# Performance work log

Hardware: AMD Instinct MI355X
Metric: run time of the kernel (lower is better)

Reference implementation:

```python
import jax, jax.numpy as jnp
import numpy as np

N_NODES = 20000
N_EDGES = 320000
MUL = 64            # multiplicity of 0e and 1o node irreps
N_SPECIES = 5
N_BESSEL = 8
RAD_HIDDEN = 64
N_TP_W = 4 * MUL    # 4 uvu paths, 64 weights each
AVG_NEIGH = 16.0
SQ3 = np.sqrt(3.0).astype(np.float32)


def setup_inputs() -> dict:
    key = jax.random.key(0)
    ks = jax.random.split(key, 16)
    inp = {
        'node_feats': jax.random.normal(ks[0], (N_NODES, 4 * MUL), jnp.float32),
        'node_attrs': jax.random.uniform(ks[1], (N_NODES, N_SPECIES), jnp.float32),
        'edge_sh': jax.random.normal(ks[2], (N_EDGES, 4), jnp.float32),
        'senders': jax.random.randint(ks[3], (N_EDGES,), 0, N_NODES),
        'receivers': jax.random.randint(ks[4], (N_EDGES,), 0, N_NODES),
        'edge_embedded': jax.random.normal(ks[5], (N_EDGES, N_BESSEL), jnp.float32),
        # Linear on node feats (per-irrep mixing): 64x0e->64x0e, 64x1o->64x1o
        'Wl0': jax.random.normal(ks[6], (MUL, MUL), jnp.float32),
        'Wl1': jax.random.normal(ks[7], (MUL, MUL), jnp.float32),
        # radial MLP: 8 -> 64 -> 64 -> 256, no bias, scalar_mlp_std = 4.0
        'Wm1': jax.random.normal(ks[8], (N_BESSEL, RAD_HIDDEN), jnp.float32) * 4.0,
        'Wm2': jax.random.normal(ks[9], (RAD_HIDDEN, RAD_HIDDEN), jnp.float32) * 4.0,
        'Wm3': jax.random.normal(ks[10], (RAD_HIDDEN, N_TP_W), jnp.float32) * 4.0,
        # output Linear: (128x0e + 128x1o after TP) -> h_out (128x0e + 64x1o)
        'W2s': jax.random.normal(ks[11], (2 * MUL, 2 * MUL), jnp.float32),
        'W2v': jax.random.normal(ks[12], (2 * MUL, MUL), jnp.float32),
        # residual FullyConnectedTensorProduct(node_feats, node_attrs) -> h_out
        'Wr_s': jax.random.normal(ks[13], (MUL, N_SPECIES, 2 * MUL), jnp.float32),
        'Wr_v': jax.random.normal(ks[14], (MUL, N_SPECIES, MUL), jnp.float32),
    }
    return inp


def reference(node_feats, node_attrs, edge_sh, senders, receivers, edge_embedded,
              Wl0, Wl1, Wm1, Wm2, Wm3, W2s, W2v, Wr_s, Wr_v):
    N = node_feats.shape[0]
    x0 = node_feats[:, :MUL]                       # [N, 64]   0e scalars
    x1 = node_feats[:, MUL:].reshape(N, MUL, 3)    # [N, 64, 3] 1o vectors

    # --- residual FullyConnectedTensorProduct(node_feats, node_attrs) -> h_out ---
    # node_attrs are 0e scalars: paths 0e x 0e -> 0e and 1o x 0e -> 1o.
    nr = 1.0 / np.sqrt(MUL * N_SPECIES).astype(np.float32)  # fan-in norm
    res_s = jnp.einsum('nu,ns,usv->nv', x0, node_attrs, Wr_s) * nr   # [N, 128]
    res_v = jnp.einsum('num,ns,usv->nvm', x1, node_attrs, Wr_v) * nr # [N, 64, 3]

    # --- Linear(node_feats.irreps) ---
    nl = 1.0 / np.sqrt(MUL).astype(np.float32)
    y0 = (x0 @ Wl0) * nl                                  # [N, 64]
    y1 = jnp.einsum('num,uv->nvm', x1, Wl1) * nl          # [N, 64, 3]

    # --- gather to edges ---
    e0 = y0[senders]          # [E, 64]
    e1 = y1[senders]          # [E, 64, 3]
    sh0 = edge_sh[:, 0]       # [E]
    sh1 = edge_sh[:, 1:4]     # [E, 3]

    # --- radial MLP producing per-edge TP weights ---
    h = jax.nn.swish(edge_embedded @ Wm1 / np.sqrt(N_BESSEL, dtype=np.float32))
    h = jax.nn.swish(h @ Wm2 / np.sqrt(RAD_HIDDEN, dtype=np.float32))
    w = h @ Wm3 / np.sqrt(RAD_HIDDEN, dtype=np.float32)   # [E, 256]
    w1, w2, w3, w4 = (w[:, :MUL], w[:, MUL:2*MUL], w[:, 2*MUL:3*MUL], w[:, 3*MUL:])

    # --- equivariant tensor product (uvu), 4 paths ---
    # 0e x 0e -> 0e ; 1o x 1o -> 0e (CG = delta/sqrt(3))
    tp_s = jnp.concatenate([
        w1 * e0 * sh0[:, None],
        w4 * jnp.einsum('eum,em->eu', e1, sh1) / SQ3,
    ], axis=1)  # [E, 128]
    # 0e x 1o -> 1o ; 1o x 0e -> 1o
    tp_v = jnp.concatenate([
        w2[:, :, None] * e0[:, :, None] * sh1[:, None, :],
        w3[:, :, None] * e1 * sh0[:, None, None],
    ], axis=1)  # [E, 128, 3]

    # --- scatter-sum aggregation over receivers ---
    agg_s = jax.ops.segment_sum(tp_s, receivers, num_segments=N) / AVG_NEIGH          # [N, 128]
    agg_v = jax.ops.segment_sum(tp_v.reshape(-1, 2 * MUL * 3), receivers,
                                num_segments=N).reshape(N, 2 * MUL, 3) / AVG_NEIGH    # [N, 128, 3]

    # --- Linear(h_out_irreps) ---
    n2 = 1.0 / np.sqrt(2 * MUL).astype(np.float32)
    z_s = (agg_s @ W2s) * n2                               # [N, 128] (64 scalars + 64 gates)
    z_v = jnp.einsum('num,uv->nvm', agg_v, W2v) * n2       # [N, 64, 3]

    # residual connection
    z_s = z_s + res_s
    z_v = z_v + res_v

    # --- gate: even_act = swish on scalars and gate scalars; gated 1o vectors ---
    out_s = jax.nn.swish(z_s[:, :MUL])                     # [N, 64]
    gates = jax.nn.swish(z_s[:, MUL:])                     # [N, 64]
    out_v = gates[:, :, None] * z_v                        # [N, 64, 3]

    return jnp.concatenate([out_s, out_v.reshape(N, MUL * 3)], axis=1)  # [N, 256]
```

## Files before the change

### kernel.cpp

```cpp
#include <hip/hip_runtime.h>
#include <hip/hip_fp16.h>


#define NN 20000
#define NE 320000

typedef _Float16 h2v __attribute__((ext_vector_type(2)));
typedef _Float16 f16x8 __attribute__((ext_vector_type(8)));
typedef float f32x4 __attribute__((ext_vector_type(4)));

__device__ __forceinline__ float swishf(float x) {
  float t = __expf(-fabsf(x));
  float r = 1.0f / (1.0f + t);
  float sig = (x >= 0.0f) ? r : t * r;
  return x * sig;
}

__device__ __forceinline__ unsigned pack2h(float a, float b) {
  __half2 h = __floats2half2_rn(a, b);
  return *reinterpret_cast<unsigned*>(&h);
}

__device__ __forceinline__ h2v u32h2(unsigned u) {
  union { unsigned u; h2v h; } x; x.u = u; return x.h;
}

__device__ __forceinline__ h2v packh2v(float a, float b) {
  h2v h; h.x = (_Float16)a; h.y = (_Float16)b; return h;
}

__device__ __forceinline__ f16x8 u4f16(uint4 u) {
  union { uint4 u; f16x8 h; } x; x.u = u; return x.h;
}

__device__ __forceinline__ void ld8(float d[8], const float* p) {
  float4 a0 = *(const float4*)p;
  float4 a1 = *(const float4*)(p + 4);
  d[0]=a0.x; d[1]=a0.y; d[2]=a0.z; d[3]=a0.w;
  d[4]=a1.x; d[5]=a1.y; d[6]=a1.z; d[7]=a1.w;
}

__device__ __forceinline__ void fma8v(float (&acc)[8], const float* p, float w) {
  float4 a0 = *(const float4*)p;
  float4 a1 = *(const float4*)(p + 4);
  acc[0] = fmaf(a0.x, w, acc[0]); acc[1] = fmaf(a0.y, w, acc[1]);
  acc[2] = fmaf(a0.z, w, acc[2]); acc[3] = fmaf(a0.w, w, acc[3]);
  acc[4] = fmaf(a1.x, w, acc[4]); acc[5] = fmaf(a1.y, w, acc[5]);
  acc[6] = fmaf(a1.z, w, acc[6]); acc[7] = fmaf(a1.w, w, acc[7]);
}

__global__ __launch_bounds__(256) void hist_kernel(const int* __restrict__ rcv,
                                                   int* __restrict__ counts) {
  int e = blockIdx.x * 256 + threadIdx.x;
  atomicAdd(&counts[rcv[e]], 1);
}

__global__ __launch_bounds__(1024) void scan_kernel(const int* __restrict__ counts,
                                                    int* __restrict__ offsets,
                                                    int* __restrict__ cursor) {
  __shared__ int part[1024];
  const int t = threadIdx.x;
  const int base = t * 20;
  int loc[20];
  int s = 0;
  #pragma unroll
  for (int j = 0; j < 20; ++j) {
    int idx = base + j;
    int c = (idx < NN) ? counts[idx] : 0;
    loc[j] = s;
    s += c;
  }
  part[t] = s;
  __syncthreads();
  for (int d = 1; d < 1024; d <<= 1) {
    int v = (t >= d) ? part[t - d] : 0;
    __syncthreads();
    part[t] += v;
    __syncthreads();
  }
  int excl = (t > 0) ? part[t - 1] : 0;
  #pragma unroll
  for (int j = 0; j < 20; ++j) {
    int idx = base + j;
    if (idx < NN) {
      int o = excl + loc[j];
      offsets[idx] = o;
      cursor[idx] = o;
    }
  }
  if (t == 1023) offsets[NN] = part[1023];
}

__global__ __launch_bounds__(256) void scatter_full(
    const int* __restrict__ rcv, const int* __restrict__ snd,
    const float* __restrict__ esh, int* __restrict__ cursor,
    int* __restrict__ csr_edge, int* __restrict__ snd_sorted,
    float* __restrict__ sh_sorted) {
  int e = blockIdx.x * 256 + threadIdx.x;
  int r = rcv[e];
  int pos = atomicAdd(&cursor[r], 1);
  csr_edge[pos] = e;
  snd_sorted[pos] = snd[e];
  float4 sh = *(const float4*)(esh + (size_t)e * 4);
  *(float4*)(sh_sorted + (size_t)pos * 4) = sh;
}

__global__ __launch_bounds__(256) void scatter_kernel(
    const int* __restrict__ rcv, int* __restrict__ cursor,
    int* __restrict__ csr_edge) {
  int e = blockIdx.x * 256 + threadIdx.x;
  int r = rcv[e];
  int pos = atomicAdd(&cursor[r], 1);
  csr_edge[pos] = e;
}

__global__ __launch_bounds__(256) void pack_weights(
    const float* __restrict__ Wm2, const float* __restrict__ Wm3,
    unsigned* __restrict__ Wm2P, unsigned* __restrict__ Wm3P,
    unsigned* __restrict__ Wm3T) {
  int idx = blockIdx.x * 256 + threadIdx.x;
  if (idx < 2048) {
    int k2 = idx >> 6, v = idx & 63;
    Wm2P[idx] = pack2h(Wm2[(2 * k2) * 64 + v], Wm2[(2 * k2 + 1) * 64 + v]);
  } else if (idx < 10240) {
    int r = idx - 2048;
    int k2 = r >> 8, c = r & 255;
    Wm3P[r] = pack2h(Wm3[(2 * k2) * 256 + c], Wm3[(2 * k2 + 1) * 256 + c]);
  } else if (idx < 18432) {
    int r = idx - 10240;
    int c = r >> 5, j = r & 31;
    Wm3T[r] = pack2h(Wm3[(2 * j) * 256 + c], Wm3[(2 * j + 1) * 256 + c]);
  }
}

__global__ __launch_bounds__(256) void pack_node_B(
    const float* __restrict__ Wr_s, const float* __restrict__ W2s,
    const float* __restrict__ Wr_v, const float* __restrict__ W2v,
    unsigned* __restrict__ BsT, unsigned* __restrict__ BvT) {
  const float nr = 0.05590169943749474f;
  const float n2 = 0.08838834764831845f;
  int idx = blockIdx.x * 256 + threadIdx.x;
  if (idx < 28672) {
    int v = idx / 224, j = idx % 224;
    float a, b;
    if (j < 160) {
      int s = j >> 5, u0 = (j & 31) << 1;
      a = Wr_s[(u0 * 5 + s) * 128 + v] * nr;
      b = Wr_s[((u0 + 1) * 5 + s) * 128 + v] * nr;
    } else {
      int c0 = (j - 160) << 1;
      a = W2s[c0 * 128 + v] * n2;
      b = W2s[(c0 + 1) * 128 + v] * n2;
    }
    BsT[idx] = pack2h(a, b);
  } else if (idx < 43008) {
    int r = idx - 28672;
    int v = r / 224, j = r % 224;
    float a, b;
    if (j < 160) {
      int s = j >> 5, u0 = (j & 31) << 1;
      a = Wr_v[(u0 * 5 + s) * 64 + v] * nr;
      b = Wr_v[((u0 + 1) * 5 + s) * 64 + v] * nr;
    } else {
      int c0 = (j - 160) << 1;
      a = W2v[c0 * 64 + v] * n2;
      b = W2v[(c0 + 1) * 64 + v] * n2;
    }
    BvT[r] = pack2h(a, b);
  }
}

__global__ __launch_bounds__(256) void node_prep(
    const float* __restrict__ feats, const float* __restrict__ Wl0,
    const float* __restrict__ Wl1, float* __restrict__ y)
{
  __shared__ __align__(16) float sX[4 * 256];
  const int t = threadIdx.x;
  const int n0 = blockIdx.x * 4;
  #pragma unroll
  for (int nb = 0; nb < 4; ++nb)
    sX[nb * 256 + t] = feats[(size_t)(n0 + nb) * 256 + t];
  __syncthreads();

  float acc[4] = {0.f, 0.f, 0.f, 0.f};
  if (t < 64) {
    const int v = t;
    for (int u = 0; u < 64; ++u) {
      float w = Wl0[u * 64 + v];
      acc[0] = fmaf(sX[0 * 256 + u], w, acc[0]);
      acc[1] = fmaf(sX[1 * 256 + u], w, acc[1]);
      acc[2] = fmaf(sX[2 * 256 + u], w, acc[2]);
      acc[3] = fmaf(sX[3 * 256 + u], w, acc[3]);
    }
  } else {
    const int i = t - 64;
    const int v = i / 3;
    const int m = i - v * 3;
    for (int u = 0; u < 64; ++u) {
      float w = Wl1[u * 64 + v];
      int xi = 64 + u * 3 + m;
      acc[0] = fmaf(sX[0 * 256 + xi], w, acc[0]);
      acc[1] = fmaf(sX[1 * 256 + xi], w, acc[1]);
      acc[2] = fmaf(sX[2 * 256 + xi], w, acc[2]);
      acc[3] = fmaf(sX[3 * 256 + xi], w, acc[3]);
    }
  }
  #pragma unroll
  for (int nb = 0; nb < 4; ++nb)
    y[(size_t)(n0 + nb) * 256 + t] = acc[nb] * 0.125f;
}

__device__ __forceinline__ void wgemv(float (&wa)[64], const float* __restrict__ Wm3,
                                      const float* h2col, int p)
{
  #pragma unroll
  for (int v = 0; v < 64; ++v) wa[v] = 0.f;
  #pragma unroll 2
  for (int k = 0; k < 64; ++k) {
    float h2k = h2col[k * 256];
    const float* wrow = Wm3 + k * 256 + p * 64;
    #pragma unroll
    for (int v = 0; v < 64; ++v) wa[v] = fmaf(h2k, wrow[v], wa[v]);
  }
}

__global__ __launch_bounds__(256, 4) void w_kernel(
    const int* __restrict__ csr_edge, const float* __restrict__ emb,
    const float* __restrict__ Wm1, const unsigned* __restrict__ Wm2P,
    const unsigned* __restrict__ Wm3T, __half* __restrict__ w_sorted)
{
  __shared__ unsigned sA[256 * 32];
  const int tid = threadIdx.x;
  const int i = blockIdx.x * 256 + tid;
  const int e = csr_edge[i];

  float e8[8];
  ld8(e8, emb + (size_t)e * 8);
  float h2a[64];
  #pragma unroll
  for (int v = 0; v < 64; ++v) h2a[v] = 0.f;
  #pragma unroll 1
  for (int k2 = 0; k2 < 32; ++k2) {
    float a0 = 0.f, a1 = 0.f;
    #pragma unroll
    for (int j = 0; j < 8; ++j) {
      a0 = fmaf(e8[j], Wm1[j * 64 + 2 * k2], a0);
      a1 = fmaf(e8[j], Wm1[j * 64 + 2 * k2 + 1], a1);
    }
    h2v ph = packh2v(swishf(a0 * 0.35355339059327373f),
                     swishf(a1 * 0.35355339059327373f));
    const unsigned* wrow = Wm2P + k2 * 64;
    #pragma unroll
    for (int v = 0; v < 64; ++v)
      h2a[v] = __builtin_amdgcn_fdot2(ph, u32h2(wrow[v]), h2a[v], false);
  }
  {
    const int r = tid;
    #pragma unroll
    for (int c = 0; c < 8; ++c) {
      uint4 v;
      v.x = pack2h(swishf(h2a[8 * c + 0] * 0.125f), swishf(h2a[8 * c + 1] * 0.125f));
      v.y = pack2h(swishf(h2a[8 * c + 2] * 0.125f), swishf(h2a[8 * c + 3] * 0.125f));
      v.z = pack2h(swishf(h2a[8 * c + 4] * 0.125f), swishf(h2a[8 * c + 5] * 0.125f));
      v.w = pack2h(swishf(h2a[8 * c + 6] * 0.125f), swishf(h2a[8 * c + 7] * 0.125f));
      *(uint4*)&sA[r * 32 + ((c ^ (r & 7)) << 2)] = v;
    }
  }
  __syncthreads();

  const int l = tid & 63;
  const int wv = tid >> 6;
  const int lg = l >> 4;
  const int lm = l & 15;

  f16x8 bfr[4][2];
  #pragma unroll
  for (int nt = 0; nt < 4; ++nt) {
    int row = wv * 64 + nt * 16 + lm;
    #pragma unroll
    for (int kh = 0; kh < 2; ++kh) {
      uint4 u = *(const uint4*)&sA[row * 32 + ((((kh << 2) + lg) ^ (row & 7)) << 2)];
      bfr[nt][kh] = u4f16(u);
    }
  }
  unsigned* sTw = sA + wv * 2048;
  const int eb = blockIdx.x * 256 + wv * 64;

  #pragma unroll 1
  for (int p = 0; p < 4; ++p) {
    #pragma unroll
    for (int mtl = 0; mtl < 4; ++mtl) {
      const int mt = p * 4 + mtl;
      int arow = mt * 16 + lm;
      uint4 u0 = *(const uint4*)&Wm3T[arow * 32 + (lg << 2)];
      uint4 u1 = *(const uint4*)&Wm3T[arow * 32 + 16 + (lg << 2)];
      f16x8 a0 = u4f16(u0), a1 = u4f16(u1);
      #pragma unroll
      for (int nt = 0; nt < 4; ++nt) {
        f32x4 acc = {0.f, 0.f, 0.f, 0.f};
        acc = __builtin_amdgcn_mfma_f32_16x16x32_f16(a0, bfr[nt][0], acc, 0, 0, 0);
        acc = __builtin_amdgcn_mfma_f32_16x16x32_f16(a1, bfr[nt][1], acc, 0, 0, 0);
        const int r = nt * 16 + lm;
        const int u = mtl * 4 + lg;
        const int pos8 = ((((u >> 1) ^ (r & 7)) << 1) | (u & 1));
        uint2 pk;
        pk.x = pack2h(acc[0], acc[1]);
        pk.y = pack2h(acc[2], acc[3]);
        *(uint2*)&sTw[r * 32 + pos8 * 2] = pk;
      }
    }
    #pragma unroll
    for (int g = 0; g < 8; ++g) {
      const int er = g * 8 + (l >> 3);
      const int c8 = l & 7;
      uint4 v = *(const uint4*)&sTw[er * 32 + ((c8 ^ (er & 7)) << 2)];
      *(uint4*)(w_sorted + (size_t)(eb + er) * 256 + p * 64 + c8 * 8) = v;
    }
  }
}

__global__ __launch_bounds__(256) void gather_tp(
    const float* __restrict__ y, const __half* __restrict__ w_sorted,
    const float* __restrict__ sh_sorted, const int* __restrict__ snd_sorted,
    const int* __restrict__ offsets, float* __restrict__ agg)
{
  const int l = threadIdx.x & 63;
  const int wv = threadIdx.x >> 6;
  const int n = blockIdx.x * 4 + wv;
  const int row0 = offsets[n];
  const int row1 = offsets[n + 1];

  float s0 = 0.f, s1 = 0.f;
  float v0x = 0.f, v0y = 0.f, v0z = 0.f;
  float v1x = 0.f, v1y = 0.f, v1z = 0.f;

  for (int i = row0; i < row1; ++i) {
    const int s = snd_sorted[i];
    const float4 sh = *(const float4*)(sh_sorted + (size_t)i * 4);
    const __half* wr = w_sorted + (size_t)i * 256;
    float w1 = __half2float(wr[l]);
    float w2 = __half2float(wr[64 + l]);
    float w3 = __half2float(wr[128 + l]);
    float w4 = __half2float(wr[192 + l]);
    const float* yr = y + (size_t)s * 256;
    float e0 = yr[l];
    float ex = yr[64 + 3 * l], ey = yr[65 + 3 * l], ez = yr[66 + 3 * l];

    s0 = fmaf(w1 * e0, sh.x, s0);
    s1 = fmaf(w4, fmaf(ex, sh.y, fmaf(ey, sh.z, ez * sh.w)), s1);
    float t2 = w2 * e0;
    v0x = fmaf(t2, sh.y, v0x); v0y = fmaf(t2, sh.z, v0y); v0z = fmaf(t2, sh.w, v0z);
    float t3 = w3 * sh.x;
    v1x = fmaf(t3, ex, v1x); v1y = fmaf(t3, ey, v1y); v1z = fmaf(t3, ez, v1z);
  }

  const float SCL = 0.0078125f;
  const float C4  = 0.125f / (16.0f * 1.7320508075688772f);
  float* ar = agg + (size_t)n * 512;
  ar[l]       = s0 * SCL;
  ar[64 + l]  = s1 * C4;
  ar[128 + 3 * l]     = v0x * SCL;
  ar[128 + 3 * l + 1] = v0y * SCL;
  ar[128 + 3 * l + 2] = v0z * SCL;
  ar[320 + 3 * l]     = v1x * SCL;
  ar[320 + 3 * l + 1] = v1y * SCL;
  ar[320 + 3 * l + 2] = v1z * SCL;
}

__global__ __launch_bounds__(256) void node_gemm(
    const float* __restrict__ feats, const float* __restrict__ attrs,
    const float* __restrict__ agg, const unsigned* __restrict__ BsT,
    const unsigned* __restrict__ BvT, float* __restrict__ out)
{
  __shared__ unsigned sAK[64 * 224];
  __shared__ float sX[16 * 257];
  __shared__ float sAt[16 * 5];
  const int t = threadIdx.x;
  const int n0 = blockIdx.x * 16;

  float* zsL = sX;
  __half* zvL = (__half*)(sX + 2048);

  #pragma unroll
  for (int nb = 0; nb < 16; ++nb)
    sX[nb * 257 + t] = feats[(size_t)(n0 + nb) * 256 + t];
  if (t < 80) sAt[t] = attrs[(size_t)n0 * 5 + t];
  __syncthreads();

  {
    const int row = t >> 2;
    const int part = t & 3;
    const bool is_s = row < 16;
    int node, m = 0;
    if (is_s) node = row;
    else { int vi = row - 16; node = vi / 3; m = vi - node * 3; }
    const float* xrow = &sX[node * 257];
    const float* atr = &sAt[node * 5];
    const float* aggr = agg + (size_t)(n0 + node) * 512;
    unsigned* arow = &sAK[row * 224];
    #pragma unroll 8
    for (int jj = 0; jj < 56; ++jj) {
      const int j = part + 4 * jj;
      float v0, v1;
      if (jj < 40) {
        int s = j >> 5;
        int u0 = (j & 31) << 1;
        float a = atr[s];
        float x0 = is_s ? xrow[u0]     : xrow[64 + 3 * u0 + m];
        float x1 = is_s ? xrow[u0 + 1] : xrow[64 + 3 * u0 + 3 + m];
        v0 = x0 * a;
        v1 = x1 * a;
      } else {
        int c0 = (j - 160) << 1;
        if (is_s) { v0 = aggr[c0]; v1 = aggr[c0 + 1]; }
        else {
          v0 = aggr[128 + 3 * c0 + m];
          v1 = aggr[128 + 3 * c0 + 3 + m];
        }
      }
      int chs = (jj & ~7) | ((jj ^ row) & 7);
      arow[(chs << 2) + part] = pack2h(v0, v1);
    }
  }
  __syncthreads();

  const int l = t & 63;
  const int wv = t >> 6;
  const int lm = l & 15;
  const int lg = l >> 4;

  #pragma unroll 1
  for (int jj = 0; jj < 5; ++jj) {
    const int jd = wv + 4 * jj;
    int mtile, ntile;
    const unsigned* Bt;
    if (jd < 8) { mtile = 0; ntile = jd; Bt = BsT; }
    else { int q = jd - 8; mtile = 1 + (q >> 2); ntile = q & 3; Bt = BvT; }

    const int arow0 = mtile * 16 + lm;
    const unsigned* brow = Bt + (ntile * 16 + lm) * 224;

    uint4 ubr[14];
    #pragma unroll
    for (int ks = 0; ks < 14; ++ks)
      ubr[ks] = *(const uint4*)&brow[(ks * 4 + lg) << 2];

    f32x4 acc = {0.f, 0.f, 0.f, 0.f};
    #pragma unroll
    for (int ks = 0; ks < 14; ++ks) {
      int ch = ks * 4 + lg;
      int chs = (ch & ~7) | ((ch ^ arow0) & 7);
      uint4 ua = *(const uint4*)&sAK[arow0 * 224 + (chs << 2)];
      acc = __builtin_amdgcn_mfma_f32_16x16x32_f16(u4f16(ua), u4f16(ubr[ks]), acc, 0, 0, 0);
    }
    const int drow = mtile * 16 + lg * 4;
    if (jd < 8) {
      #pragma unroll
      for (int rr = 0; rr < 4; ++rr)
        zsL[(drow + rr) * 128 + ntile * 16 + lm] = acc[rr];
    } else {
      const int vi0 = drow - 16;
      #pragma unroll
      for (int rr = 0; rr < 4; ++rr)
        zvL[(vi0 + rr) * 64 + ntile * 16 + lm] = __float2half(acc[rr]);
    }
  }
  __syncthreads();

  int ug = 0, mg = 0;
  if (t >= 64) { ug = (t - 64) / 3; mg = (t - 64) - ug * 3; }
  #pragma unroll 4
  for (int nb = 0; nb < 16; ++nb) {
    float val;
    if (t < 64) {
      val = swishf(zsL[nb * 128 + t]);
    } else {
      float gate = swishf(zsL[nb * 128 + 64 + ug]);
      val = gate * __half2float(zvL[(nb * 3 + mg) * 64 + ug]);
    }
    out[(size_t)(n0 + nb) * 256 + t] = val;
  }
}

__global__ __launch_bounds__(512, 2) void gather_fused(
    const float* __restrict__ y, const int* __restrict__ csr_edge,
    const int* __restrict__ snd, const float* __restrict__ esh,
    const float* __restrict__ emb, const float* __restrict__ Wm1,
    const float* __restrict__ Wm2, const float* __restrict__ Wm3,
    const int* __restrict__ offsets, float* __restrict__ agg)
{
  __shared__ __align__(16) float sW3[64 * 256];
  __shared__ __align__(16) float sH[8 * 4 * 64];
  const int t = threadIdx.x;

  #pragma unroll 4
  for (int i = 0; i < 32; ++i) {
    int idx = i * 512 + t;
    int k = idx >> 8;
    int c = idx & 255;
    float v = Wm3[idx];
    int kg = k >> 2, kk = k & 3;
    sW3[c * 64 + (((kg ^ (c & 15)) & 15) << 2) + kk] = v;
  }
  __syncthreads();

  const int l = t & 63;
  const int wv = t >> 6;
  const int n = blockIdx.x * 8 + wv;
  const int row0 = offsets[n];
  const int row1 = offsets[n + 1];

  float* sHw = &sH[wv * 256];

  float wm1r[8];
  #pragma unroll
  for (int j = 0; j < 8; ++j) wm1r[j] = Wm1[j * 64 + l];

  float s0 = 0.f, s1 = 0.f;
  float v0x = 0.f, v0y = 0.f, v0z = 0.f;
  float v1x = 0.f, v1y = 0.f, v1z = 0.f;

  const int swz = ((l & 15) << 2);

  for (int i = row0; i < row1; i += 4) {
    const int nb = row1 - i;

    int   sn[4];
    float4 sh[4];
    #pragma unroll
    for (int b = 0; b < 4; ++b) {
      int idx = (b < nb) ? (i + b) : i;
      int e = csr_edge[idx];
      sn[b] = snd[e];
      float4 s = *(const float4*)(esh + (size_t)e * 4);
      if (b >= nb) s = make_float4(0.f, 0.f, 0.f, 0.f);
      sh[b] = s;
      float em8[8];
      ld8(em8, emb + (size_t)e * 8);
      float a = 0.f;
      #pragma unroll
      for (int j = 0; j < 8; ++j) a = fmaf(em8[j], wm1r[j], a);
      sHw[b * 64 + l] = swishf(a * 0.35355339059327373f);
    }

    float h2[4] = {0.f, 0.f, 0.f, 0.f};
    #pragma unroll 4
    for (int q = 0; q < 16; ++q) {
      float wq0 = Wm2[(4 * q + 0) * 64 + l];
      float wq1 = Wm2[(4 * q + 1) * 64 + l];
      float wq2 = Wm2[(4 * q + 2) * 64 + l];
      float wq3 = Wm2[(4 * q + 3) * 64 + l];
      #pragma unroll
      for (int b = 0; b < 4; ++b) {
        float4 h = *(const float4*)&sHw[b * 64 + 4 * q];
        h2[b] = fmaf(h.x, wq0, h2[b]);
        h2[b] = fmaf(h.y, wq1, h2[b]);
        h2[b] = fmaf(h.z, wq2, h2[b]);
        h2[b] = fmaf(h.w, wq3, h2[b]);
      }
    }
    #pragma unroll
    for (int b = 0; b < 4; ++b)
      h2[b] = swishf(h2[b] * 0.125f);
    #pragma unroll
    for (int b = 0; b < 4; ++b)
      sHw[b * 64 + l] = h2[b];

    float w0[4]  = {0,0,0,0}, w1a[4] = {0,0,0,0};
    float w2a[4] = {0,0,0,0}, w3a[4] = {0,0,0,0};
    #pragma unroll 1
    for (int g = 0; g < 16; ++g) {
      int sbase = l * 64 + (((g << 2) ^ swz) & 63);
      float4 m0 = *(const float4*)&sW3[sbase];
      float4 m1 = *(const float4*)&sW3[sbase + 4096];
      float4 m2 = *(const float4*)&sW3[sbase + 8192];
      float4 m3 = *(const float4*)&sW3[sbase + 12288];
      #pragma unroll
      for (int b = 0; b < 4; ++b) {
        float4 hb = *(const float4*)&sHw[b * 64 + 4 * g];
        #pragma unroll
        for (int kk = 0; kk < 4; ++kk) {
          float bc = (&hb.x)[kk];
          w0[b]  = fmaf(bc, (&m0.x)[kk], w0[b]);
          w1a[b] = fmaf(bc, (&m1.x)[kk], w1a[b]);
          w2a[b] = fmaf(bc, (&m2.x)[kk], w2a[b]);
          w3a[b] = fmaf(bc, (&m3.x)[kk], w3a[b]);
        }
      }
    }

    #pragma unroll
    for (int b = 0; b < 4; ++b) {
      const float* yr = y + (size_t)sn[b] * 256;
      float e0 = yr[l];
      float ex = yr[64 + 3 * l], ey = yr[65 + 3 * l], ez = yr[66 + 3 * l];
      float4 s = sh[b];
      s0 = fmaf(w0[b] * e0, s.x, s0);
      s1 = fmaf(w3a[b], fmaf(ex, s.y, fmaf(ey, s.z, ez * s.w)), s1);
      float t2 = w1a[b] * e0;
      v0x = fmaf(t2, s.y, v0x); v0y = fmaf(t2, s.z, v0y); v0z = fmaf(t2, s.w, v0z);
      float t3 = w2a[b] * s.x;
      v1x = fmaf(t3, ex, v1x); v1y = fmaf(t3, ey, v1y); v1z = fmaf(t3, ez, v1z);
    }
  }

  const float SCL = 0.0078125f;
  const float C4  = 0.125f / (16.0f * 1.7320508075688772f);
  float* ar = agg + (size_t)n * 512;
  ar[l]       = s0 * SCL;
  ar[64 + l]  = s1 * C4;
  ar[128 + 3 * l]     = v0x * SCL;
  ar[128 + 3 * l + 1] = v0y * SCL;
  ar[128 + 3 * l + 2] = v0z * SCL;
  ar[320 + 3 * l]     = v1x * SCL;
  ar[320 + 3 * l + 1] = v1y * SCL;
  ar[320 + 3 * l + 2] = v1z * SCL;
}

__global__ __launch_bounds__(256) void edge_kernel(
    const float* __restrict__ y, const float* __restrict__ edge_sh,
    const int* __restrict__ senders, const int* __restrict__ receivers,
    const float* __restrict__ emb, const float* __restrict__ Wm1,
    const float* __restrict__ Wm2, const float* __restrict__ Wm3,
    float* __restrict__ agg)
{
  __shared__ float h2s[64 * 256];
  const int tid = threadIdx.x;
  const int e = blockIdx.x * 256 + tid;
  const int s = senders[e];
  const int r = receivers[e];
  const float4 shv = *(const float4*)(edge_sh + (size_t)e * 4);
  float e8[8];
  ld8(e8, emb + (size_t)e * 8);

  float h2a[64];
  #pragma unroll
  for (int v = 0; v < 64; ++v) h2a[v] = 0.f;
  #pragma unroll 2
  for (int k = 0; k < 64; ++k) {
    float a = 0.f;
    #pragma unroll
    for (int j = 0; j < 8; ++j) a = fmaf(e8[j], Wm1[j * 64 + k], a);
    float h1k = swishf(a * 0.35355339059327373f);
    const float* wrow = Wm2 + k * 64;
    #pragma unroll
    for (int v = 0; v < 64; ++v) h2a[v] = fmaf(h1k, wrow[v], h2a[v]);
  }
  #pragma unroll
  for (int v = 0; v < 64; ++v)
    h2s[v * 256 + tid] = swishf(h2a[v] * 0.125f);

  const float* yrow = y + (size_t)s * 256;
  float* aggr = agg + (size_t)r * 512;
  const float SCL = 0.0078125f;
  const float c0  = shv.x * SCL;
  const float c1x = shv.y * SCL, c1y = shv.z * SCL, c1z = shv.w * SCL;
  const float c4  = 0.125f / (16.0f * 1.7320508075688772f);

  float wa[64];

  wgemv(wa, Wm3, h2s + tid, 0);
  #pragma unroll
  for (int uc = 0; uc < 8; ++uc) {
    float ev[8];
    ld8(ev, yrow + uc * 8);
    #pragma unroll
    for (int j = 0; j < 8; ++j) {
      int u = uc * 8 + j;
      atomicAdd(&aggr[u], wa[u] * ev[j] * c0);
    }
  }
  wgemv(wa, Wm3, h2s + tid, 1);
  #pragma unroll
  for (int uc = 0; uc < 8; ++uc) {
    float ev[8];
    ld8(ev, yrow + uc * 8);
    #pragma unroll
    for (int j = 0; j < 8; ++j) {
      int u = uc * 8 + j;
      float tt = wa[u] * ev[j];
      atomicAdd(&aggr[128 + 3 * u    ], tt * c1x);
      atomicAdd(&aggr[128 + 3 * u + 1], tt * c1y);
      atomicAdd(&aggr[128 + 3 * u + 2], tt * c1z);
    }
  }
  wgemv(wa, Wm3, h2s + tid, 2);
  #pragma unroll
  for (int uc = 0; uc < 8; ++uc) {
    float ev[24];
    ld8(ev,      yrow + 64 + uc * 24);
    ld8(ev + 8,  yrow + 64 + uc * 24 + 8);
    ld8(ev + 16, yrow + 64 + uc * 24 + 16);
    #pragma unroll
    for (int j = 0; j < 8; ++j) {
      int u = uc * 8 + j;
      float tt = wa[u] * c0;
      atomicAdd(&aggr[320 + 3 * u    ], tt * ev[3 * j    ]);
      atomicAdd(&aggr[320 + 3 * u + 1], tt * ev[3 * j + 1]);
      atomicAdd(&aggr[320 + 3 * u + 2], tt * ev[3 * j + 2]);
    }
  }
  wgemv(wa, Wm3, h2s + tid, 3);
  #pragma unroll
  for (int uc = 0; uc < 8; ++uc) {
    float ev[24];
    ld8(ev,      yrow + 64 + uc * 24);
    ld8(ev + 8,  yrow + 64 + uc * 24 + 8);
    ld8(ev + 16, yrow + 64 + uc * 24 + 16);
    #pragma unroll
    for (int j = 0; j < 8; ++j) {
      int u = uc * 8 + j;
      float d = ev[3*j]*shv.y + ev[3*j+1]*shv.z + ev[3*j+2]*shv.w;
      atomicAdd(&aggr[64 + u], wa[u] * d * c4);
    }
  }
}

__global__ __launch_bounds__(256) void node_post(
    const float* __restrict__ feats, const float* __restrict__ attrs,
    const float* __restrict__ agg, const float* __restrict__ W2s,
    const float* __restrict__ W2v, const float* __restrict__ Wr_s,
    const float* __restrict__ Wr_v, float* __restrict__ out)
{
  __shared__ __align__(16) float sA[320 * 8];
  __shared__ __align__(16) float sX0[64 * 8];
  __shared__ __align__(16) float sX1[192 * 8];
  __shared__ __align__(16) float sAt[5 * 8];
  __shared__ __align__(16) float sAggS[128 * 8];
  __shared__ __align__(16) float sAggV[384 * 8];
  __shared__ __align__(16) float sZs[8 * 128];
  __shared__ __align__(16) float sZv[8 * 192];

  const int t = threadIdx.x;
  const int n0 = blockIdx.x * 8;
  const float nr = 0.05590169943749474f;
  const float n2 = 0.08838834764831845f;

  #pragma unroll
  for (int nb = 0; nb < 8; ++nb) {
    float v = feats[(size_t)(n0 + nb) * 256 + t];
    if (t < 64) sX0[t * 8 + nb] = v;
    else        sX1[(t - 64) * 8 + nb] = v;
  }
  if (t < 40) {
    int nb = t & 7, s = t >> 3;
    sAt[s * 8 + nb] = attrs[(size_t)(n0 + nb) * 5 + s] * nr;
  }
  #pragma unroll
  for (int i = 0; i < 16; ++i) {
    int idx = i * 256 + t;
    int nb = idx >> 9;
    int c = idx & 511;
    float v = agg[(size_t)(n0 + nb) * 512 + c] * n2;
    if (c < 128) sAggS[c * 8 + nb] = v;
    else         sAggV[(c - 128) * 8 + nb] = v;
  }
  __syncthreads();

  #pragma unroll
  for (int i = 0; i < 10; ++i) {
    int idx = i * 256 + t;
    int nb = idx & 7;
    int us = idx >> 3;
    int u = us / 5;
    int s = us - u * 5;
    sA[us * 8 + nb] = sX0[u * 8 + nb] * sAt[s * 8 + nb];
  }
  __syncthreads();

  float av[8][3];

  if (t < 128) {
    const int v = t;
    float acc[8];
    #pragma unroll
    for (int nb = 0; nb < 8; ++nb) acc[nb] = 0.f;
    for (int us = 0; us < 320; ++us)
      fma8v(acc, &sA[us * 8], Wr_s[us * 128 + v]);
    for (int c = 0; c < 128; ++c)
      fma8v(acc, &sAggS[c * 8], W2s[c * 128 + v]);
    #pragma unroll
    for (int nb = 0; nb < 8; ++nb) sZs[nb * 128 + v] = acc[nb];
  } else {
    const int tv = t - 128;
    const int v = tv & 63;
    const int half = tv >> 6;
    #pragma unroll
    for (int nb = 0; nb < 8; ++nb)
      #pragma unroll
      for (int m = 0; m < 3; ++m) av[nb][m] = 0.f;

    const int u0 = half * 32;
    for (int u = u0; u < u0 + 32; ++u) {
      float xr0[8], xr1[8], xr2[8];
      ld8(xr0, &sX1[(u * 3 + 0) * 8]);
      ld8(xr1, &sX1[(u * 3 + 1) * 8]);
      ld8(xr2, &sX1[(u * 3 + 2) * 8]);
      #pragma unroll
      for (int s = 0; s < 5; ++s) {
        float w = Wr_v[(u * 5 + s) * 64 + v];
        float at[8];
        ld8(at, &sAt[s * 8]);
        #pragma unroll
        for (int nb = 0; nb < 8; ++nb) {
          float tt = at[nb] * w;
          av[nb][0] = fmaf(xr0[nb], tt, av[nb][0]);
          av[nb][1] = fmaf(xr1[nb], tt, av[nb][1]);
          av[nb][2] = fmaf(xr2[nb], tt, av[nb][2]);
        }
      }
    }
    const int c0 = half * 64;
    for (int c = c0; c < c0 + 64; ++c) {
      float w = W2v[c * 64 + v];
      float g0[8], g1[8], g2[8];
      ld8(g0, &sAggV[(c * 3 + 0) * 8]);
      ld8(g1, &sAggV[(c * 3 + 1) * 8]);
      ld8(g2, &sAggV[(c * 3 + 2) * 8]);
      #pragma unroll
      for (int nb = 0; nb < 8; ++nb) {
        av[nb][0] = fmaf(g0[nb], w, av[nb][0]);
        av[nb][1] = fmaf(g1[nb], w, av[nb][1]);
        av[nb][2] = fmaf(g2[nb], w, av[nb][2]);
      }
    }
    if (half == 0) {
      #pragma unroll
      for (int nb = 0; nb < 8; ++nb)
        #pragma unroll
        for (int m = 0; m < 3; ++m)
          sZv[nb * 192 + v * 3 + m] = av[nb][m];
    }
  }
  __syncthreads();
  if (t >= 192) {
    const int v = (t - 128) & 63;
    #pragma unroll
    for (int nb = 0; nb < 8; ++nb)
      #pragma unroll
      for (int m = 0; m < 3; ++m)
        sZv[nb * 192 + v * 3 + m] += av[nb][m];
  }
  __syncthreads();

  const int i = t - 64;
  const int ug = (t >= 64) ? (i / 3) : 0;
  #pragma unroll
  for (int nb = 0; nb < 8; ++nb) {
    float val;
    if (t < 64) {
      val = swishf(sZs[nb * 128 + t]);
    } else {
      float gate = swishf(sZs[nb * 128 + 64 + ug]);
      val = gate * sZv[nb * 192 + i];
    }
    out[(size_t)(n0 + nb) * 256 + t] = val;
  }
}

extern "C" void kernel_launch(void* const* d_in, const int* in_sizes, int n_in,
                              void* d_out, int out_size, void* d_ws, size_t ws_size,
                              hipStream_t stream)
{
  const float* feats = (const float*)d_in[0];
  const float* attrs = (const float*)d_in[1];
  const float* esh   = (const float*)d_in[2];
  const int*   snd   = (const int*)d_in[3];
  const int*   rcv   = (const int*)d_in[4];
  const float* emb   = (const float*)d_in[5];
  const float* Wl0   = (const float*)d_in[6];
  const float* Wl1   = (const float*)d_in[7];
  const float* Wm1   = (const float*)d_in[8];
  const float* Wm2   = (const float*)d_in[9];
  const float* Wm3   = (const float*)d_in[10];
  const float* W2s   = (const float*)d_in[11];
  const float* W2v   = (const float*)d_in[12];
  const float* Wr_s  = (const float*)d_in[13];
  const float* Wr_v  = (const float*)d_in[14];
  float* out = (float*)d_out;

  float* y   = (float*)d_ws;
  float* agg = y + (size_t)NN * 256;
  int* counts = (int*)agg;
  int* cursor = counts + NN;
  int* csr_edge = (int*)(agg + (size_t)NN * 512);
  int* offsets  = csr_edge + NE;
  int* snd_sorted = offsets + NN + 1;
  float* sh_sorted = (float*)(snd_sorted + NE);
  __half* w_sorted = (__half*)(sh_sorted + (size_t)NE * 4);
  unsigned* Wm2P = (unsigned*)(w_sorted + (size_t)NE * 256);
  unsigned* Wm3P = Wm2P + 2048;
  unsigned* Wm3T = Wm3P + 8192;
  unsigned* BsT  = Wm3T + 8192;
  unsigned* BvT  = BsT + 28672;
  size_t need1 = (size_t)((char*)(BvT + 14336) - (char*)d_ws);
  size_t need2 = (size_t)((char*)(offsets + NN + 1) - (char*)d_ws);

  if (ws_size >= need1) {
    hipMemsetAsync(counts, 0, (size_t)NN * sizeof(int), stream);
    hist_kernel<<<NE / 256, 256, 0, stream>>>(rcv, counts);
    scan_kernel<<<1, 1024, 0, stream>>>(counts, offsets, cursor);
    scatter_full<<<NE / 256, 256, 0, stream>>>(rcv, snd, esh, cursor,
                                               csr_edge, snd_sorted, sh_sorted);
    pack_weights<<<72, 256, 0, stream>>>(Wm2, Wm3, Wm2P, Wm3P, Wm3T);
    pack_node_B<<<168, 256, 0, stream>>>(Wr_s, W2s, Wr_v, W2v, BsT, BvT);
    node_prep<<<NN / 4, 256, 0, stream>>>(feats, Wl0, Wl1, y);
    w_kernel<<<NE / 256, 256, 0, stream>>>(csr_edge, emb, Wm1, Wm2P, Wm3T, w_sorted);
    gather_tp<<<NN / 4, 256, 0, stream>>>(y, w_sorted, sh_sorted, snd_sorted,
                                          offsets, agg);
    node_gemm<<<NN / 16, 256, 0, stream>>>(feats, attrs, agg, BsT, BvT, out);
  } else if (ws_size >= need2) {
    hipMemsetAsync(counts, 0, (size_t)NN * sizeof(int), stream);
    hist_kernel<<<NE / 256, 256, 0, stream>>>(rcv, counts);
    scan_kernel<<<1, 1024, 0, stream>>>(counts, offsets, cursor);
    scatter_kernel<<<NE / 256, 256, 0, stream>>>(rcv, cursor, csr_edge);
    node_prep<<<NN / 4, 256, 0, stream>>>(feats, Wl0, Wl1, y);
    gather_fused<<<NN / 8, 512, 0, stream>>>(y, csr_edge, snd, esh, emb,
                                             Wm1, Wm2, Wm3, offsets, agg);
    node_post<<<NN / 8, 256, 0, stream>>>(feats, attrs, agg, W2s, W2v, Wr_s, Wr_v, out);
  } else {
    hipMemsetAsync(agg, 0, (size_t)NN * 512 * sizeof(float), stream);
    node_prep<<<NN / 4, 256, 0, stream>>>(feats, Wl0, Wl1, y);
    edge_kernel<<<NE / 256, 256, 0, stream>>>(y, esh, snd, rcv, emb, Wm1, Wm2, Wm3, agg);
    node_post<<<NN / 8, 256, 0, stream>>>(feats, attrs, agg, W2s, W2v, Wr_s, Wr_v, out);
  }
}
```

Measured before the change: 342.3 us.

## Split node GEMM K dimension into two halves to cut shared memory and change agg layout

The node_gemm kernel now builds the fp16 A operand in two K-halves of 112 channels, reusing a smaller shared buffer and keeping five accumulators in registers across the halves. Node features are read straight from global memory instead of being staged in shared memory. The gather kernel stores aggregated vectors component-major (x, y, z planes) so the GEMM reads agg contiguously. The goal is lower LDS use for higher occupancy and coalesced agg access, at the cost of an extra barrier pair and uncoalesced strided global reads of feats.

After: 337.5 us. Within noise of the previous version (-1.4%).

```diff
diff --git a/kernel.cpp b/kernel.cpp
--- a/kernel.cpp
+++ b/kernel.cpp
@@ -359,12 +359,12 @@
   float* ar = agg + (size_t)n * 512;
   ar[l]       = s0 * SCL;
   ar[64 + l]  = s1 * C4;
-  ar[128 + 3 * l]     = v0x * SCL;
-  ar[128 + 3 * l + 1] = v0y * SCL;
-  ar[128 + 3 * l + 2] = v0z * SCL;
-  ar[320 + 3 * l]     = v1x * SCL;
-  ar[320 + 3 * l + 1] = v1y * SCL;
-  ar[320 + 3 * l + 2] = v1z * SCL;
+  ar[128 + l]        = v0x * SCL;
+  ar[128 + 64 + l]   = v1x * SCL;
+  ar[256 + l]        = v0y * SCL;
+  ar[256 + 64 + l]   = v1y * SCL;
+  ar[384 + l]        = v0z * SCL;
+  ar[384 + 64 + l]   = v1z * SCL;
 }
 
 __global__ __launch_bounds__(256) void node_gemm(
@@ -372,56 +372,14 @@
     const float* __restrict__ agg, const unsigned* __restrict__ BsT,
     const unsigned* __restrict__ BvT, float* __restrict__ out)
 {
-  __shared__ unsigned sAK[64 * 224];
-  __shared__ float sX[16 * 257];
+  __shared__ unsigned sAK[64 * 128];
+  __shared__ float zsL[16 * 128];
+  __shared__ __half zvL[48 * 64];
   __shared__ float sAt[16 * 5];
   const int t = threadIdx.x;
   const int n0 = blockIdx.x * 16;
 
-  float* zsL = sX;
-  __half* zvL = (__half*)(sX + 2048);
-
-  #pragma unroll
-  for (int nb = 0; nb < 16; ++nb)
-    sX[nb * 257 + t] = feats[(size_t)(n0 + nb) * 256 + t];
   if (t < 80) sAt[t] = attrs[(size_t)n0 * 5 + t];
-  __syncthreads();
-
-  {
-    const int row = t >> 2;
-    const int part = t & 3;
-    const bool is_s = row < 16;
-    int node, m = 0;
-    if (is_s) node = row;
-    else { int vi = row - 16; node = vi / 3; m = vi - node * 3; }
-    const float* xrow = &sX[node * 257];
-    const float* atr = &sAt[node * 5];
-    const float* aggr = agg + (size_t)(n0 + node) * 512;
-    unsigned* arow = &sAK[row * 224];
-    #pragma unroll 8
-    for (int jj = 0; jj < 56; ++jj) {
-      const int j = part + 4 * jj;
-      float v0, v1;
-      if (jj < 40) {
-        int s = j >> 5;
-        int u0 = (j & 31) << 1;
-        float a = atr[s];
-        float x0 = is_s ? xrow[u0]     : xrow[64 + 3 * u0 + m];
-        float x1 = is_s ? xrow[u0 + 1] : xrow[64 + 3 * u0 + 3 + m];
-        v0 = x0 * a;
-        v1 = x1 * a;
-      } else {
-        int c0 = (j - 160) << 1;
-        if (is_s) { v0 = aggr[c0]; v1 = aggr[c0 + 1]; }
-        else {
-          v0 = aggr[128 + 3 * c0 + m];
-          v1 = aggr[128 + 3 * c0 + 3 + m];
-        }
-      }
-      int chs = (jj & ~7) | ((jj ^ row) & 7);
-      arow[(chs << 2) + part] = pack2h(v0, v1);
-    }
-  }
   __syncthreads();
 
   const int l = t & 63;
@@ -429,40 +387,95 @@
   const int lm = l & 15;
   const int lg = l >> 4;
 
+  f32x4 acc[5];
+  #pragma unroll
+  for (int jj = 0; jj < 5; ++jj) acc[jj] = (f32x4){0.f, 0.f, 0.f, 0.f};
+
   #pragma unroll 1
+  for (int h = 0; h < 2; ++h) {
+    {
+      const int row = t >> 2;
+      const int part = t & 3;
+      const bool is_s = row < 16;
+      int node, m = 0;
+      if (is_s) node = row;
+      else { int vi = row - 16; node = vi / 3; m = vi - node * 3; }
+      const float* xrow = feats + (size_t)(n0 + node) * 256;
+      const float* atr = &sAt[node * 5];
+      const float* aggr = agg + (size_t)(n0 + node) * 512;
+      unsigned* arow = &sAK[row * 128];
+      #pragma unroll 7
+      for (int jj = 0; jj < 28; ++jj) {
+        const int jl = part + 4 * jj;
+        const int jg = h * 112 + jl;
+        float v0, v1;
+        if (jg < 160) {
+          int s = jg >> 5;
+          int u0 = (jg & 31) << 1;
+          float a = atr[s];
+          float x0 = is_s ? xrow[u0]     : xrow[64 + 3 * u0 + m];
+          float x1 = is_s ? xrow[u0 + 1] : xrow[64 + 3 * u0 + 3 + m];
+          v0 = x0 * a;
+          v1 = x1 * a;
+        } else {
+          int c0 = (jg - 160) << 1;
+          if (is_s) { v0 = aggr[c0]; v1 = aggr[c0 + 1]; }
+          else {
+            v0 = aggr[128 + m * 128 + c0];
+            v1 = aggr[128 + m * 128 + c0 + 1];
+          }
+        }
+        int chs = (jj & ~7) | ((jj ^ row) & 7);
+        arow[(chs << 2) + part] = pack2h(v0, v1);
+      }
+    }
+    __syncthreads();
+
+    #pragma unroll
+    for (int jj = 0; jj < 5; ++jj) {
+      const int jd = wv + 4 * jj;
+      int mtile, ntile;
+      const unsigned* Bt;
+      if (jd < 8) { mtile = 0; ntile = jd; Bt = BsT; }
+      else { int q = jd - 8; mtile = 1 + (q >> 2); ntile = q & 3; Bt = BvT; }
+
+      const int arow0 = mtile * 16 + lm;
+      const unsigned* brow = Bt + (ntile * 16 + lm) * 224 + h * 112;
+
+      uint4 ubr[7];
+      #pragma unroll
+      for (int ks = 0; ks < 7; ++ks)
+        ubr[ks] = *(const uint4*)&brow[(ks * 4 + lg) << 2];
+
+      f32x4 a = acc[jj];
+      #pragma unroll
+      for (int ks = 0; ks < 7; ++ks) {
+        int ch = ks * 4 + lg;
+        int chs = (ch & ~7) | ((ch ^ arow0) & 7);
+        uint4 ua = *(const uint4*)&sAK[arow0 * 128 + (chs << 2)];
+        a = __builtin_amdgcn_mfma_f32_16x16x32_f16(u4f16(ua), u4f16(ubr[ks]), a, 0, 0, 0);
+      }
+      acc[jj] = a;
+    }
+    __syncthreads();
+  }
+
+  #pragma unroll
   for (int jj = 0; jj < 5; ++jj) {
     const int jd = wv + 4 * jj;
     int mtile, ntile;
-    const unsigned* Bt;
-    if (jd < 8) { mtile = 0; ntile = jd; Bt = BsT; }
-    else { int q = jd - 8; mtile = 1 + (q >> 2); ntile = q & 3; Bt = BvT; }
-
-    const int arow0 = mtile * 16 + lm;
-    const unsigned* brow = Bt + (ntile * 16 + lm) * 224;
-
-    uint4 ubr[14];
-    #pragma unroll
-    for (int ks = 0; ks < 14; ++ks)
-      ubr[ks] = *(const uint4*)&brow[(ks * 4 + lg) << 2];
-
-    f32x4 acc = {0.f, 0.f, 0.f, 0.f};
-    #pragma unroll
-    for (int ks = 0; ks < 14; ++ks) {
-      int ch = ks * 4 + lg;
-      int chs = (ch & ~7) | ((ch ^ arow0) & 7);
-      uint4 ua = *(const uint4*)&sAK[arow0 * 224 + (chs << 2)];
-      acc = __builtin_amdgcn_mfma_f32_16x16x32_f16(u4f16(ua), u4f16(ubr[ks]), acc, 0, 0, 0);
-    }
+    if (jd < 8) { mtile = 0; ntile = jd; }
+    else { int q = jd - 8; mtile = 1 + (q >> 2); ntile = q & 3; }
     const int drow = mtile * 16 + lg * 4;
     if (jd < 8) {
       #pragma unroll
       for (int rr = 0; rr < 4; ++rr)
-        zsL[(drow + rr) * 128 + ntile * 16 + lm] = acc[rr];
+        zsL[(drow + rr) * 128 + ntile * 16 + lm] = acc[jj][rr];
     } else {
       const int vi0 = drow - 16;
       #pragma unroll
       for (int rr = 0; rr < 4; ++rr)
-        zvL[(vi0 + rr) * 64 + ntile * 16 + lm] = __float2half(acc[rr]);
+        zvL[(vi0 + rr) * 64 + ntile * 16 + lm] = __float2half(acc[jj][rr]);
     }
   }
   __syncthreads();
```
